# Kernel tuning notes

Hardware: AMD Instinct MI355X
Metric: run time of the kernel (lower is better)

The kernel has to match this reference:

```python
import jax, jax.numpy as jnp
import numpy as np

H, K_CHUNKS = 16, 16          # z_num = (h, k)
Z_DIM = 64
OC, IC, KW = 128, 128, 3      # per-chunk out, in, kernel width
HID = 256
O, I = H * OC, K_CHUNKS * IC  # 2048, 2048
L = 3
N_PDE, D_PDE = 1024, 64


def setup_inputs() -> dict:
    key = jax.random.key(0)
    ks = jax.random.split(key, 10)
    def rn(k, shape, scale=1.0):
        return jax.random.normal(k, shape, dtype=jnp.float32) * scale
    return {
        "Z": rn(ks[0], (H * K_CHUNKS, Z_DIM)),                 # stacked z_list (fmod(randn,2) ~ randn)
        "z_bias": rn(ks[1], (O,)),
        "unet_1d_weights": rn(ks[2], (O, I, L), 0.02),
        "unet_1d_bias": rn(ks[3], (O,), 0.02),
        "pde_inputs": rn(ks[4], (N_PDE, D_PDE)),
        "W1": rn(ks[5], (Z_DIM, HID), 1.0 / np.sqrt(Z_DIM)),
        "U1": rn(ks[6], (D_PDE, HID), 1.0 / np.sqrt(D_PDE)),
        "b1": jnp.zeros((HID,), jnp.float32),
        "W2": rn(ks[7], (HID, OC * IC * KW), 1.0 / np.sqrt(HID)),
        "b2": jnp.zeros((OC * IC * KW,), jnp.float32),
    }


def reference(Z, z_bias, unet_1d_weights, unet_1d_bias, pde_inputs, W1, U1, b1, W2, b2):
    # Batched hypernet: replaces the h*k sequential hyper_net calls.
    pde_feat = pde_inputs.mean(axis=0) @ U1                    # [HID], shared conditioning
    hidden = jnp.tanh(Z @ W1 + pde_feat + b1)                  # [h*k, HID]
    w = (hidden @ W2 + b2).reshape(H, K_CHUNKS, OC, IC, KW)    # per-chunk weights
    # cat over j along dim=1 (in-channels), then over i along dim=0 (out-channels)
    exe_unet_weight = w.transpose(0, 2, 1, 3, 4).reshape(O, I, KW)  # [O, I, K]
    w_2d = jnp.einsum('oik,oil->oikl', exe_unet_weight, unet_1d_weights)  # [O, I, K, L]
    bb = z_bias + unet_1d_bias                                 # [O]
    return (w_2d, bb)
```

## Files before the change

kernel.cpp:

```cpp
#include <hip/hip_runtime.h>
#include <hip/hip_bf16.h>
#include <math.h>

#define H_ 16
#define KC_ 16
#define ZD_ 64
#define OC_ 128
#define IC_ 128
#define KW_ 3
#define HID_ 256
#define O_ 2048
#define I_ 2048
#define NW2_ 49152
#define W2D_OUT (O_ * I_ * KW_ * 3)

typedef short bf16x8 __attribute__((ext_vector_type(8)));
typedef float f32x4 __attribute__((ext_vector_type(4)));

static __device__ __forceinline__ unsigned short f2bf(float f) {
    union { float f; unsigned u; } v; v.f = f;
    unsigned r = v.u + 0x7FFF + ((v.u >> 16) & 1);
    return (unsigned short)(r >> 16);
}

__global__ void prep_kernel(const float* __restrict__ Z,
                            const float* __restrict__ pde,
                            const float* __restrict__ W1,
                            const float* __restrict__ U1,
                            const float* __restrict__ b1,
                            const float* __restrict__ z_bias,
                            const float* __restrict__ u_bias,
                            unsigned short* __restrict__ hidden_bf,
                            float* __restrict__ out_bb) {
    __shared__ float part[16][64];
    __shared__ float meanv[64];
    __shared__ float zr[64];
    const int t = threadIdx.x, m = blockIdx.x;
    if (t < 64) zr[t] = Z[m * ZD_ + t];
    const int c4 = t & 15, rg = t >> 4;
    float sx = 0.f, sy = 0.f, sz = 0.f, sw = 0.f;
    const float4* p = (const float4*)pde;
    for (int r = 0; r < 64; ++r) {
        float4 v = p[(rg * 64 + r) * 16 + c4];
        sx += v.x; sy += v.y; sz += v.z; sw += v.w;
    }
    part[rg][c4 * 4 + 0] = sx; part[rg][c4 * 4 + 1] = sy;
    part[rg][c4 * 4 + 2] = sz; part[rg][c4 * 4 + 3] = sw;
    __syncthreads();
    if (t < 64) {
        float a = 0.f;
        #pragma unroll
        for (int g = 0; g < 16; ++g) a += part[g][t];
        meanv[t] = a * (1.f / 1024.f);
    }
    __syncthreads();
    float f = b1[t];
    #pragma unroll
    for (int d = 0; d < 64; ++d) f = fmaf(meanv[d], U1[d * HID_ + t], f);
    float s = f;
    #pragma unroll
    for (int d = 0; d < 64; ++d) s = fmaf(zr[d], W1[d * HID_ + t], s);
    hidden_bf[m * HID_ + t] = f2bf(tanhf(s));
    if (m < 8) {
        const int idx = m * 256 + t;
        out_bb[idx] = z_bias[idx] + u_bias[idx];
    }
}

__global__ __launch_bounds__(256, 4)
void gemm_expand(const unsigned short* __restrict__ hidden_bf,
                 const float* __restrict__ W2,
                 const float* __restrict__ b2,
                 const float* __restrict__ unet,
                 float* __restrict__ out) {
    __shared__ unsigned short bT[384 * 40];

    const int t = threadIdx.x;
    const int lane = t & 63;
    const int wave = t >> 6;
    const int oc = blockIdx.x >> 3;
    const int hp = blockIdx.x & 7;
    const int h = hp * 2 + (wave & 1);
    const int wn0 = (wave >> 1) * 192;
    const int n15 = lane & 15;
    const int quad = lane >> 4;
    const int n0g = oc * 384;
    const int kg = wave;

    f32x4 acc[12];
    #pragma unroll
    for (int i = 0; i < 12; ++i) acc[i] = (f32x4){0.f, 0.f, 0.f, 0.f};

    const unsigned short* arow = hidden_bf + (h * 16 + n15) * HID_;

    for (int c = 0; c < 8; ++c) {
        #pragma unroll
        for (int it = 0; it < 6; ++it) {
            const int n = it * 64 + lane;
            const float* src = W2 + (size_t)(c * 32 + kg * 8) * NW2_ + n0g + n;
            unsigned short u8[8];
            #pragma unroll
            for (int jj = 0; jj < 8; ++jj)
                u8[jj] = f2bf(src[(size_t)jj * NW2_]);
            *(bf16x8*)&bT[n * 40 + kg * 8] = *(bf16x8*)u8;
        }
        __syncthreads();
        const bf16x8 a = *(const bf16x8*)(arow + c * 32 + quad * 8);
        #pragma unroll
        for (int nt = 0; nt < 12; ++nt) {
            const bf16x8 bfr = *(const bf16x8*)&bT[(wn0 + nt * 16 + n15) * 40 + quad * 8];
            acc[nt] = __builtin_amdgcn_mfma_f32_16x16x32_bf16(a, bfr, acc[nt], 0, 0, 0);
        }
        __syncthreads();
    }

    const int o = h * 128 + oc;
    const size_t obase = (size_t)o * 18432;
    const size_t ubase = (size_t)o * 6144;
    #pragma unroll
    for (int nt = 0; nt < 12; ++nt) {
        const int n_rel = wn0 + nt * 16 + n15;
        const int ic = (n_rel * 171) >> 9;
        const float gb2 = b2[n0g + n_rel];
        #pragma unroll
        for (int r = 0; r < 4; ++r) {
            const int kc = quad * 4 + r;
            const float w = acc[nt][r] + gb2;
            const float* ub = unet + ubase + kc * 384 + ic * 3;
            float* ob = out + obase + kc * 1152 + n_rel * 3;
            ob[0] = w * ub[0];
            ob[1] = w * ub[1];
            ob[2] = w * ub[2];
        }
    }
}

extern "C" void kernel_launch(void* const* d_in, const int* in_sizes, int n_in,
                              void* d_out, int out_size, void* d_ws, size_t ws_size,
                              hipStream_t stream) {
    const float* Z       = (const float*)d_in[0];
    const float* z_bias  = (const float*)d_in[1];
    const float* unet_w  = (const float*)d_in[2];
    const float* unet_b  = (const float*)d_in[3];
    const float* pde     = (const float*)d_in[4];
    const float* W1      = (const float*)d_in[5];
    const float* U1      = (const float*)d_in[6];
    const float* b1      = (const float*)d_in[7];
    const float* W2      = (const float*)d_in[8];
    const float* b2      = (const float*)d_in[9];
    float* out = (float*)d_out;

    unsigned short* hidden_bf = (unsigned short*)d_ws;

    prep_kernel<<<256, 256, 0, stream>>>(Z, pde, W1, U1, b1, z_bias, unet_b,
                                         hidden_bf, out + W2D_OUT);
    gemm_expand<<<1024, 256, 0, stream>>>(hidden_bf, W2, b2, unet_w, out);
}
```

Baseline: 330.5 us.

## Retile hypernet GEMM so each block covers all heads for a column slice

The GEMM block now spans all 16 heads (M=256) for a 96-column slice of W2, so each W2 element is loaded and converted to bf16 only once instead of once per head pair. W2 is read with float4 loads and transposed into LDS, and hidden is stored in a K-chunked layout so A fragments load contiguously from global memory. The epilogue writes triples through a 12-byte struct. Blocks grow to 512 threads and the grid halves, which changes occupancy and per-wave register use.

```diff
diff --git a/kernel.cpp b/kernel.cpp
--- a/kernel.cpp
+++ b/kernel.cpp
@@ -5,17 +5,16 @@
 #define H_ 16
 #define KC_ 16
 #define ZD_ 64
-#define OC_ 128
-#define IC_ 128
-#define KW_ 3
 #define HID_ 256
 #define O_ 2048
-#define I_ 2048
 #define NW2_ 49152
-#define W2D_OUT (O_ * I_ * KW_ * 3)
+#define W2D_OUT 37748736
+#define DPDE_ 64
 
 typedef short bf16x8 __attribute__((ext_vector_type(8)));
 typedef float f32x4 __attribute__((ext_vector_type(4)));
+
+struct F3 { float x, y, z; };
 
 static __device__ __forceinline__ unsigned short f2bf(float f) {
     union { float f; unsigned u; } v; v.f = f;
@@ -30,7 +29,7 @@
                             const float* __restrict__ b1,
                             const float* __restrict__ z_bias,
                             const float* __restrict__ u_bias,
-                            unsigned short* __restrict__ hidden_bf,
+                            unsigned short* __restrict__ hiddenA,
                             float* __restrict__ out_bb) {
     __shared__ float part[16][64];
     __shared__ float meanv[64];
@@ -60,77 +59,87 @@
     float s = f;
     #pragma unroll
     for (int d = 0; d < 64; ++d) s = fmaf(zr[d], W1[d * HID_ + t], s);
-    hidden_bf[m * HID_ + t] = f2bf(tanhf(s));
+    hiddenA[((size_t)(t >> 3) * 256 + m) * 8 + (t & 7)] = f2bf(tanhf(s));
     if (m < 8) {
         const int idx = m * 256 + t;
         out_bb[idx] = z_bias[idx] + u_bias[idx];
     }
 }
 
-__global__ __launch_bounds__(256, 4)
-void gemm_expand(const unsigned short* __restrict__ hidden_bf,
+__global__ __launch_bounds__(512, 4)
+void gemm_expand(const unsigned short* __restrict__ hiddenA,
                  const float* __restrict__ W2,
                  const float* __restrict__ b2,
                  const float* __restrict__ unet,
                  float* __restrict__ out) {
-    __shared__ unsigned short bT[384 * 40];
+    __shared__ unsigned short bT[96 * 72];
 
     const int t = threadIdx.x;
     const int lane = t & 63;
     const int wave = t >> 6;
-    const int oc = blockIdx.x >> 3;
-    const int hp = blockIdx.x & 7;
-    const int h = hp * 2 + (wave & 1);
-    const int wn0 = (wave >> 1) * 192;
     const int n15 = lane & 15;
     const int quad = lane >> 4;
-    const int n0g = oc * 384;
-    const int kg = wave;
+    const int oc = blockIdx.x >> 2;
+    const int icq = blockIdx.x & 3;
+    const int n0g = oc * 384 + icq * 96;
 
-    f32x4 acc[12];
+    f32x4 acc[2][6];
     #pragma unroll
-    for (int i = 0; i < 12; ++i) acc[i] = (f32x4){0.f, 0.f, 0.f, 0.f};
+    for (int a = 0; a < 2; ++a)
+        #pragma unroll
+        for (int b = 0; b < 6; ++b) acc[a][b] = (f32x4){0.f, 0.f, 0.f, 0.f};
 
-    const unsigned short* arow = hidden_bf + (h * 16 + n15) * HID_;
-
-    for (int c = 0; c < 8; ++c) {
+    for (int c = 0; c < 4; ++c) {
         #pragma unroll
-        for (int it = 0; it < 6; ++it) {
-            const int n = it * 64 + lane;
-            const float* src = W2 + (size_t)(c * 32 + kg * 8) * NW2_ + n0g + n;
-            unsigned short u8[8];
-            #pragma unroll
-            for (int jj = 0; jj < 8; ++jj)
-                u8[jj] = f2bf(src[(size_t)jj * NW2_]);
-            *(bf16x8*)&bT[n * 40 + kg * 8] = *(bf16x8*)u8;
+        for (int i = 0; i < 3; ++i) {
+            const int e = i * 512 + t;
+            const int kk = e / 24;
+            const int nq = e - kk * 24;
+            const float4 v = *(const float4*)(W2 + (size_t)(c * 64 + kk) * NW2_ + n0g + nq * 4);
+            unsigned short* d = &bT[(nq * 4) * 72 + kk];
+            d[0]       = f2bf(v.x);
+            d[72]      = f2bf(v.y);
+            d[144]     = f2bf(v.z);
+            d[216]     = f2bf(v.w);
         }
         __syncthreads();
-        const bf16x8 a = *(const bf16x8*)(arow + c * 32 + quad * 8);
         #pragma unroll
-        for (int nt = 0; nt < 12; ++nt) {
-            const bf16x8 bfr = *(const bf16x8*)&bT[(wn0 + nt * 16 + n15) * 40 + quad * 8];
-            acc[nt] = __builtin_amdgcn_mfma_f32_16x16x32_bf16(a, bfr, acc[nt], 0, 0, 0);
+        for (int kh = 0; kh < 2; ++kh) {
+            const int g = c * 8 + kh * 4 + quad;
+            bf16x8 afr[2];
+            #pragma unroll
+            for (int mi = 0; mi < 2; ++mi)
+                afr[mi] = *(const bf16x8*)(hiddenA +
+                          ((size_t)g * 256 + (wave * 2 + mi) * 16 + n15) * 8);
+            #pragma unroll
+            for (int nt = 0; nt < 6; ++nt) {
+                const bf16x8 bfr = *(const bf16x8*)&bT[(nt * 16 + n15) * 72 + kh * 32 + quad * 8];
+                acc[0][nt] = __builtin_amdgcn_mfma_f32_16x16x32_bf16(afr[0], bfr, acc[0][nt], 0, 0, 0);
+                acc[1][nt] = __builtin_amdgcn_mfma_f32_16x16x32_bf16(afr[1], bfr, acc[1][nt], 0, 0, 0);
+            }
         }
         __syncthreads();
     }
 
-    const int o = h * 128 + oc;
-    const size_t obase = (size_t)o * 18432;
-    const size_t ubase = (size_t)o * 6144;
     #pragma unroll
-    for (int nt = 0; nt < 12; ++nt) {
-        const int n_rel = wn0 + nt * 16 + n15;
-        const int ic = (n_rel * 171) >> 9;
-        const float gb2 = b2[n0g + n_rel];
+    for (int mi = 0; mi < 2; ++mi) {
+        const int o = (wave * 2 + mi) * 128 + oc;
+        const float* ub_o = unet + (size_t)o * 6144;
+        float* ob_o = out + (size_t)o * 18432;
         #pragma unroll
-        for (int r = 0; r < 4; ++r) {
-            const int kc = quad * 4 + r;
-            const float w = acc[nt][r] + gb2;
-            const float* ub = unet + ubase + kc * 384 + ic * 3;
-            float* ob = out + obase + kc * 1152 + n_rel * 3;
-            ob[0] = w * ub[0];
-            ob[1] = w * ub[1];
-            ob[2] = w * ub[2];
+        for (int nt = 0; nt < 6; ++nt) {
+            const int nl = nt * 16 + n15;
+            const int n_rel = icq * 96 + nl;
+            const int ic = n_rel / 3;
+            const float gb2 = b2[n0g + nl];
+            #pragma unroll
+            for (int r = 0; r < 4; ++r) {
+                const int kc = quad * 4 + r;
+                const float w = acc[mi][nt][r] + gb2;
+                const F3 u = *(const F3*)(ub_o + kc * 384 + ic * 3);
+                F3 res; res.x = w * u.x; res.y = w * u.y; res.z = w * u.z;
+                *(F3*)(ob_o + kc * 1152 + n_rel * 3) = res;
+            }
         }
     }
 }
@@ -150,9 +159,9 @@
     const float* b2      = (const float*)d_in[9];
     float* out = (float*)d_out;
 
-    unsigned short* hidden_bf = (unsigned short*)d_ws;
+    unsigned short* hiddenA = (unsigned short*)d_ws;
 
     prep_kernel<<<256, 256, 0, stream>>>(Z, pde, W1, U1, b1, z_bias, unet_b,
-                                         hidden_bf, out + W2D_OUT);
-    gemm_expand<<<1024, 256, 0, stream>>>(hidden_bf, W2, b2, unet_w, out);
+                                         hiddenA, out + W2D_OUT);
+    gemm_expand<<<512, 512, 0, stream>>>(hiddenA, W2, b2, unet_w, out);
 }
```

After: 278.9 us. -15.6%, faster.
